# Performance work log

Measured on AMD Instinct MI355X. Metric: run time of the kernel, lower is better.

The kernel has to match this reference:

```python
import jax, jax.numpy as jnp
import numpy as np

B, S, D_MODEL, N_HEAD = 8, 512, 1024, 16
HEAD_DIM = D_MODEL // N_HEAD


def _pos_embed(seq_len, dim):
    # RelativeSinusoidalPositionalEmbedding(dim, padding_idx=0, init_size=1200)
    num = 1201  # init_size + 1
    half = dim // 2
    freq = np.exp(np.arange(half, dtype=np.float32) * (-np.log(10000.0) / (half - 1)))
    pos = np.arange(-((num + 1) // 2), num // 2, dtype=np.float32)  # tf.range(-num//2, num//2), python floor div
    emb = pos[:, None] * freq[None, :]
    table = np.concatenate([np.sin(emb), np.cos(emb)], axis=1).astype(np.float32)  # [num, dim]
    table[0] = 0.0  # padding_idx = 0
    origin_shift = num // 2 + 1  # 601
    idx = np.arange(-seq_len, seq_len) + origin_shift
    return jnp.asarray(table[idx])  # [2*seq_len, dim]


def setup_inputs() -> dict:
    key = jax.random.key(0)
    k1, k2, k3, k4 = jax.random.split(key, 4)
    return {
        "x": jax.random.normal(k1, (B, S, D_MODEL), dtype=jnp.float32),
        "mask": jnp.ones((B, S), dtype=jnp.int32),
        "Wqv": jax.random.normal(k2, (D_MODEL, 2 * D_MODEL), dtype=jnp.float32) * 0.02,
        "r_r_bias": jax.random.normal(k3, (N_HEAD, HEAD_DIM), dtype=jnp.float32) * 0.02,
        "r_w_bias": jax.random.normal(k4, (N_HEAD, HEAD_DIM), dtype=jnp.float32) * 0.02,
    }


def _shift(BD):
    # [b, h, s, 2s] -> [b, h, s, s] via pad-reshape trick
    b, h, s, _ = BD.shape
    zp = jnp.zeros((b, h, s, 1), BD.dtype)
    BD = jnp.concatenate([BD, zp], axis=-1).reshape(b, h, 2 * s + 1, s)
    BD = BD[:, :, :-1].reshape(b, h, s, 2 * s)
    return BD[:, :, :, s:]


def reference(x, mask, Wqv, r_r_bias, r_w_bias):
    pos = _pos_embed(S, HEAD_DIM)  # [2S, head_dim], stop-gradient constant
    qv = x @ Wqv  # [B, S, 2*D]
    q, v = jnp.split(qv, 2, axis=-1)

    def heads(t):
        return t.reshape(B, S, N_HEAD, HEAD_DIM).transpose(0, 2, 1, 3)  # bhsd

    q, k, v = heads(q), heads(x), heads(v)
    rw_q = q + r_r_bias[None, :, None, :]
    AC = jnp.einsum('bhqd,bhkd->bhqk', rw_q, k)
    D_ = jnp.einsum('hd,ld->hl', r_w_bias, pos)[None, :, None, :]  # [1, h, 1, 2S]
    B_ = jnp.einsum('bhqd,ld->bhql', q, pos)  # [b, h, S, 2S]
    BD = _shift(B_ + D_)
    attn = AC + BD  # scale=False -> divide by 1
    m = mask.astype(jnp.float32)[:, None, None, :]
    attn = attn * m - (1.0 - m) * 1e8
    attn = jax.nn.softmax(attn, axis=-1)  # dropout is identity at inference
    out = jnp.einsum('bhqk,bhkd->bhqd', attn, v)
    return out.transpose(0, 2, 1, 3).reshape(B, S, D_MODEL)
```

## Files before the change

### kernel.cpp

```cpp
#include <hip/hip_runtime.h>


using h4 = __attribute__((ext_vector_type(4))) _Float16;
using h8 = __attribute__((ext_vector_type(8))) _Float16;
using f32x4 = __attribute__((ext_vector_type(4))) float;

#define MFMA16(a, b, c) __builtin_amdgcn_mfma_f32_16x16x32_f16((a), (b), (c), 0, 0, 0)

#define GLOAD_LDS16(gp, lp)                                                        \
  __builtin_amdgcn_global_load_lds(                                                \
      (const __attribute__((address_space(1))) unsigned int*)(gp),                 \
      (__attribute__((address_space(3))) unsigned int*)(lp), 16, 0, 0)

#define L2E 1.4426950408889634f

__global__ __launch_bounds__(256) void k_prep(const float* __restrict__ x,
                                              const float* __restrict__ Wqv,
                                              _Float16* __restrict__ xh,
                                              _Float16* __restrict__ wT,
                                              _Float16* __restrict__ posP) {
  __shared__ _Float16 t[64][72];
  int bid = blockIdx.x;
  int tid = threadIdx.x;
  if (bid < 2048) {
    size_t idx = (size_t)bid * 256 + tid;
    const float* src = x + idx * 8;
    _Float16 tmp[8];
#pragma unroll
    for (int j = 0; j < 8; ++j) tmp[j] = (_Float16)src[j];
    *(h8*)(xh + idx * 8) = *(const h8*)tmp;
  } else if (bid < 2176) {
    int idx = (bid - 2048) * 256 + tid;
    int tt = idx >> 6, j = idx & 63;
    int jj = j & 31;
    float f = expf((float)jj * (-9.210340371976184f / 31.0f));
    float ang = (float)tt * f;
    posP[idx] = (_Float16)((j < 32) ? sinf(ang) : cosf(ang));
  } else {
    int b2 = bid - 2176;
    int bk = b2 & 15, bn = b2 >> 4;
    int k0 = bk * 64, n0 = bn * 64;
    int r = tid >> 2, c = (tid & 3) * 16;
    const float* src = Wqv + (size_t)(k0 + r) * 2048 + n0 + c;
#pragma unroll
    for (int j = 0; j < 16; ++j) t[r][c + j] = (_Float16)src[j];
    __syncthreads();
    _Float16 tmp[16];
#pragma unroll
    for (int j = 0; j < 16; ++j) tmp[j] = t[c + j][r];
    _Float16* dst = wT + (size_t)(n0 + r) * 1024 + k0 + c;
    *(h8*)dst = *(const h8*)tmp;
    *(h8*)(dst + 8) = *(const h8*)(tmp + 8);
  }
}

__global__ __launch_bounds__(256) void k_gemm(const _Float16* __restrict__ xh,
                                              const _Float16* __restrict__ wT,
                                              const float* __restrict__ rr,
                                              const float* __restrict__ rw,
                                              _Float16* __restrict__ qrr,
                                              _Float16* __restrict__ qrwp,
                                              _Float16* __restrict__ vT) {
  __shared__ _Float16 At[2][128 * 64];
  __shared__ _Float16 Bt[2][128 * 64];

  int bid = blockIdx.x;
  int bm = bid & 31, bn = bid >> 5;
  int tid = threadIdx.x;
  int w = tid >> 6, lane = tid & 63;
  int lr = lane & 15, lg = lane >> 4;

  auto stage = [&](int bufi, int k0) {
#pragma unroll
    for (int it = 0; it < 4; ++it) {
      int a = w * 256 + it * 64 + lane;
      int trow = a >> 3, c8s = (a & 7) ^ (trow & 7);
      GLOAD_LDS16(xh + (size_t)(bm * 128 + trow) * 1024 + k0 + c8s * 8,
                  &At[bufi][a * 8]);
    }
#pragma unroll
    for (int it = 0; it < 4; ++it) {
      int a = w * 256 + it * 64 + lane;
      int trow = a >> 3, c8s = (a & 7) ^ (trow & 7);
      GLOAD_LDS16(wT + (size_t)(bn * 128 + trow) * 1024 + k0 + c8s * 8,
                  &Bt[bufi][a * 8]);
    }
  };

  int wm = w >> 1, wn = w & 1;
  f32x4 acc[4][4] = {};

  stage(0, 0);
  __syncthreads();
  int buf = 0;
  for (int i = 0; i < 16; ++i) {
    if (i < 15) stage(buf ^ 1, (i + 1) * 64);
#pragma unroll
    for (int kk = 0; kk < 2; ++kk) {
      h8 af[4], bf[4];
#pragma unroll
      for (int mi = 0; mi < 4; ++mi) {
        int row = wm * 64 + mi * 16 + lr;
        af[mi] = *(const h8*)(&At[buf][row * 64 + (((kk * 4 + lg) ^ (lr & 7)) * 8)]);
      }
#pragma unroll
      for (int ni = 0; ni < 4; ++ni) {
        int row = wn * 64 + ni * 16 + lr;
        bf[ni] = *(const h8*)(&Bt[buf][row * 64 + (((kk * 4 + lg) ^ (lr & 7)) * 8)]);
      }
#pragma unroll
      for (int mi = 0; mi < 4; ++mi)
#pragma unroll
        for (int ni = 0; ni < 4; ++ni)
          acc[mi][ni] = MFMA16(af[mi], bf[ni], acc[mi][ni]);
    }
    __syncthreads();
    buf ^= 1;
  }

  int hg = bn * 2 + wn;
  int mb = bm * 128 + wm * 64;
  if (hg < 16) {
    int h = hg;
    float rrv[4], rwv[4];
#pragma unroll
    for (int ni = 0; ni < 4; ++ni) {
      rrv[ni] = rr[h * 64 + ni * 16 + lr];
      rwv[ni] = rw[h * 64 + ni * 16 + lr];
    }
    float f0 = expf((float)lr * (-9.210340371976184f / 31.0f));
    float f1 = expf((float)(16 + lr) * (-9.210340371976184f / 31.0f));
#pragma unroll
    for (int mi = 0; mi < 4; ++mi)
#pragma unroll
      for (int r = 0; r < 4; ++r) {
        int m = mb + mi * 16 + lg * 4 + r;
        int b = m >> 9, s = m & 511;
        size_t base = ((size_t)(b * 16 + h) * 512 + s) * 64;
#pragma unroll
        for (int ni = 0; ni < 4; ++ni)
          qrr[base + ni * 16 + lr] = (_Float16)((acc[mi][ni][r] + rrv[ni]) * L2E);
        {
          float qs = acc[mi][0][r] + rwv[0], qc = acc[mi][2][r] + rwv[2];
          float sn, cs;
          __sincosf((float)s * f0, &sn, &cs);
          qrwp[base + lr] = (_Float16)((qs * cs + qc * sn) * L2E);
          qrwp[base + lr + 32] = (_Float16)((qc * cs - qs * sn) * L2E);
        }
        {
          float qs = acc[mi][1][r] + rwv[1], qc = acc[mi][3][r] + rwv[3];
          float sn, cs;
          __sincosf((float)s * f1, &sn, &cs);
          qrwp[base + 16 + lr] = (_Float16)((qs * cs + qc * sn) * L2E);
          qrwp[base + 16 + lr + 32] = (_Float16)((qc * cs - qs * sn) * L2E);
        }
      }
  } else {
    int h = hg - 16;
#pragma unroll
    for (int mi = 0; mi < 4; ++mi) {
      int m = mb + mi * 16 + lg * 4;
      int b = m >> 9, s0 = m & 511;
      size_t vtbase = (size_t)(b * 16 + h) * 64 * 512;
#pragma unroll
      for (int ni = 0; ni < 4; ++ni) {
        int d = ni * 16 + lr;
        _Float16 t4[4];
#pragma unroll
        for (int r = 0; r < 4; ++r) t4[r] = (_Float16)acc[mi][ni][r];
        *(h4*)(vT + vtbase + (size_t)d * 512 + s0) = *(const h4*)t4;
      }
    }
  }
}

__global__ __launch_bounds__(256, 2) void k_attn(const _Float16* __restrict__ xh,
                                                 const _Float16* __restrict__ qrr,
                                                 const _Float16* __restrict__ qrwp,
                                                 const _Float16* __restrict__ vT,
                                                 const _Float16* __restrict__ posPg,
                                                 const int* __restrict__ mask,
                                                 float* __restrict__ out) {
  __shared__ _Float16 Kp[128 * 128];
  __shared__ _Float16 Vt[64 * 128];
  __shared__ _Float16 Pl[4][16 * 136];
  __shared__ float Ma[512];

  int bid = blockIdx.x;
  int qb = bid >> 7, h = bid & 15, b = (bid >> 4) & 7;
  int q0 = qb * 128;
  int tid = threadIdx.x;
  int w = tid >> 6, lane = tid & 63;
  int lr = lane & 15, lg = lane >> 4;

  const size_t bh = (size_t)(b * 16 + h);
  const _Float16* kb = xh + (size_t)b * 512 * 1024 + h * 64;
  const _Float16* vTp = vT + bh * 64 * 512;
  const int* mrow = mask + b * 512;

  auto stage = [&](int t0s) {
#pragma unroll
    for (int it = 0; it < 8; ++it) {
      int a = w * 512 + it * 64 + lane;
      int trow = a >> 4, c16 = a & 15;
      int c16s = c16 ^ (trow & 15);
      const _Float16* g = (c16s < 8)
          ? kb + (size_t)(t0s + trow) * 1024 + c16s * 8
          : posPg + (size_t)(t0s + trow) * 64 + (c16s - 8) * 8;
      GLOAD_LDS16(g, &Kp[(size_t)(w * 512 + it * 64) * 8]);
    }
#pragma unroll
    for (int it = 0; it < 4; ++it) {
      int a = w * 256 + it * 64 + lane;
      int drow = a >> 4, c16 = a & 15;
      int c16s = c16 ^ (drow & 15);
      const _Float16* g = vTp + (size_t)drow * 512 + t0s + c16s * 8;
      GLOAD_LDS16(g, &Vt[(size_t)(w * 256 + it * 64) * 8]);
    }
  };

  Ma[tid] = (1.f - (float)mrow[tid]) * -1.4426950e8f;
  Ma[tid + 256] = (1.f - (float)mrow[tid + 256]) * -1.4426950e8f;

  h8 ar0[2], ar1[2], aw0[2], aw1[2];
#pragma unroll
  for (int rg = 0; rg < 2; ++rg) {
    const _Float16* qrr_p = qrr + (bh * 512 + q0 + 32 * w + 16 * rg + lr) * 64 + lg * 8;
    const _Float16* qrw_p = qrwp + (bh * 512 + q0 + 32 * w + 16 * rg + lr) * 64 + lg * 8;
    ar0[rg] = *(const h8*)(qrr_p);
    ar1[rg] = *(const h8*)(qrr_p + 32);
    aw0[rg] = *(const h8*)(qrw_p);
    aw1[rg] = *(const h8*)(qrw_p + 32);
  }

  float m_run[2][4], l_run[2][4];
  f32x4 O[2][4];
#pragma unroll
  for (int rg = 0; rg < 2; ++rg)
#pragma unroll
    for (int r = 0; r < 4; ++r) {
      m_run[rg][r] = -1e30f;
      l_run[rg][r] = 0.f;
      O[rg][r] = (f32x4){0.f, 0.f, 0.f, 0.f};
    }

  _Float16* pw = &Pl[w][0];

  for (int t0 = 0; t0 < 512; t0 += 128) {
    stage(t0);
    __syncthreads();

#pragma unroll
    for (int rg = 0; rg < 2; ++rg) {
      float s[8][4];
      __builtin_amdgcn_s_setprio(1);
#pragma unroll
      for (int tf = 0; tf < 8; ++tf) {
        int row = tf * 16 + lr;
        const _Float16* bp = &Kp[row * 128];
        h8 b0 = *(const h8*)(bp + ((0 + lg) ^ lr) * 8);
        h8 b1 = *(const h8*)(bp + ((4 + lg) ^ lr) * 8);
        h8 b2 = *(const h8*)(bp + ((8 + lg) ^ lr) * 8);
        h8 b3 = *(const h8*)(bp + ((12 + lg) ^ lr) * 8);
        f32x4 c = {0.f, 0.f, 0.f, 0.f};
        c = MFMA16(ar0[rg], b0, c);
        c = MFMA16(ar1[rg], b1, c);
        c = MFMA16(aw0[rg], b2, c);
        c = MFMA16(aw1[rg], b3, c);
        float ma = Ma[t0 + tf * 16 + lr];
#pragma unroll
        for (int r = 0; r < 4; ++r) s[tf][r] = c[r] + ma;
      }
      __builtin_amdgcn_s_setprio(0);

#pragma unroll
      for (int r = 0; r < 4; ++r) {
        float rm = s[0][r];
#pragma unroll
        for (int tf = 1; tf < 8; ++tf) rm = fmaxf(rm, s[tf][r]);
#pragma unroll
        for (int d = 1; d < 16; d <<= 1) rm = fmaxf(rm, __shfl_xor(rm, d));
        float mn = fmaxf(m_run[rg][r], rm);
        float sc = exp2f(m_run[rg][r] - mn);
        m_run[rg][r] = mn;
        float rs = 0.f;
#pragma unroll
        for (int tf = 0; tf < 8; ++tf) {
          float p = exp2f(s[tf][r] - mn);
          _Float16 p16 = (_Float16)p;
          pw[(lg * 4 + r) * 136 + tf * 16 + lr] = p16;
          rs += (float)p16;
        }
#pragma unroll
        for (int d = 1; d < 16; d <<= 1) rs += __shfl_xor(rs, d);
        l_run[rg][r] = l_run[rg][r] * sc + rs;
#pragma unroll
        for (int df = 0; df < 4; ++df) O[rg][df][r] *= sc;
      }

      h8 pa[4];
#pragma unroll
      for (int ks = 0; ks < 4; ++ks)
        pa[ks] = *(const h8*)(pw + lr * 136 + ks * 32 + lg * 8);
      __builtin_amdgcn_s_setprio(1);
#pragma unroll
      for (int df = 0; df < 4; ++df) {
        int row = df * 16 + lr;
        const _Float16* vbp = &Vt[row * 128];
#pragma unroll
        for (int ks = 0; ks < 4; ++ks) {
          h8 vb = *(const h8*)(vbp + ((ks * 4 + lg) ^ lr) * 8);
          O[rg][df] = MFMA16(pa[ks], vb, O[rg][df]);
        }
      }
      __builtin_amdgcn_s_setprio(0);
    }
    __syncthreads();
  }

#pragma unroll
  for (int rg = 0; rg < 2; ++rg)
#pragma unroll
    for (int df = 0; df < 4; ++df)
#pragma unroll
      for (int r = 0; r < 4; ++r) {
        int ii = 32 * w + 16 * rg + lg * 4 + r;
        out[((size_t)b * 512 + q0 + ii) * 1024 + h * 64 + df * 16 + lr] =
            O[rg][df][r] / l_run[rg][r];
      }
}

extern "C" void kernel_launch(void* const* d_in, const int* in_sizes, int n_in,
                              void* d_out, int out_size, void* d_ws, size_t ws_size,
                              hipStream_t stream) {
  const float* x = (const float*)d_in[0];
  const int* mask = (const int*)d_in[1];
  const float* Wqv = (const float*)d_in[2];
  const float* rr = (const float*)d_in[3];
  const float* rw = (const float*)d_in[4];
  float* out = (float*)d_out;
  char* ws = (char*)d_ws;
  const size_t MB = 1024 * 1024;
  _Float16* xh = (_Float16*)(ws);
  _Float16* wT = (_Float16*)(ws + 8 * MB);
  _Float16* posP = (_Float16*)(ws + 12 * MB);
  _Float16* qrr = (_Float16*)(ws + 13 * MB);
  _Float16* qrwp = (_Float16*)(ws + 21 * MB);
  _Float16* vT = (_Float16*)(ws + 29 * MB);

  k_prep<<<2688, 256, 0, stream>>>(x, Wqv, xh, wT, posP);
  k_gemm<<<512, 256, 0, stream>>>(xh, wT, rr, rw, qrr, qrwp, vT);
  k_attn<<<512, 256, 0, stream>>>(xh, qrr, qrwp, vT, posP, mask, out);
}
```

Baseline: 72.23 us.

## Transpose QK MFMA so each lane owns a query row; add lazy softmax rescale

Swaps the MFMA operands so the score tile is transposed and each lane holds one query row's scores. Row max and sum then need only two cross-lane shuffles instead of four per register. It also skips the running-max rescale of O and l unless some row's max grows by more than 8 (log2 domain), and writes P as packed h4 stores. This cuts shuffle and exp work in the softmax, but the skipped rescale risks fp16 overflow of P if the threshold is too loose.

```diff
diff --git a/kernel.cpp b/kernel.cpp
--- a/kernel.cpp
+++ b/kernel.cpp
@@ -233,16 +233,12 @@
     aw1[rg] = *(const h8*)(qrw_p + 32);
   }
 
-  float m_run[2][4], l_run[2][4];
+  float m_run[2] = {-1e30f, -1e30f}, l_run[2] = {0.f, 0.f};
   f32x4 O[2][4];
 #pragma unroll
   for (int rg = 0; rg < 2; ++rg)
 #pragma unroll
-    for (int r = 0; r < 4; ++r) {
-      m_run[rg][r] = -1e30f;
-      l_run[rg][r] = 0.f;
-      O[rg][r] = (f32x4){0.f, 0.f, 0.f, 0.f};
-    }
+    for (int df = 0; df < 4; ++df) O[rg][df] = (f32x4){0.f, 0.f, 0.f, 0.f};
 
   _Float16* pw = &Pl[w][0];
 
@@ -263,40 +259,53 @@
         h8 b2 = *(const h8*)(bp + ((8 + lg) ^ lr) * 8);
         h8 b3 = *(const h8*)(bp + ((12 + lg) ^ lr) * 8);
         f32x4 c = {0.f, 0.f, 0.f, 0.f};
-        c = MFMA16(ar0[rg], b0, c);
-        c = MFMA16(ar1[rg], b1, c);
-        c = MFMA16(aw0[rg], b2, c);
-        c = MFMA16(aw1[rg], b3, c);
-        float ma = Ma[t0 + tf * 16 + lr];
-#pragma unroll
-        for (int r = 0; r < 4; ++r) s[tf][r] = c[r] + ma;
+        c = MFMA16(b0, ar0[rg], c);
+        c = MFMA16(b1, ar1[rg], c);
+        c = MFMA16(b2, aw0[rg], c);
+        c = MFMA16(b3, aw1[rg], c);
+        f32x4 mav = *(const f32x4*)&Ma[t0 + tf * 16 + lg * 4];
+#pragma unroll
+        for (int r = 0; r < 4; ++r) s[tf][r] = c[r] + mav[r];
       }
       __builtin_amdgcn_s_setprio(0);
 
-#pragma unroll
-      for (int r = 0; r < 4; ++r) {
-        float rm = s[0][r];
-#pragma unroll
-        for (int tf = 1; tf < 8; ++tf) rm = fmaxf(rm, s[tf][r]);
-#pragma unroll
-        for (int d = 1; d < 16; d <<= 1) rm = fmaxf(rm, __shfl_xor(rm, d));
-        float mn = fmaxf(m_run[rg][r], rm);
-        float sc = exp2f(m_run[rg][r] - mn);
-        m_run[rg][r] = mn;
-        float rs = 0.f;
-#pragma unroll
-        for (int tf = 0; tf < 8; ++tf) {
-          float p = exp2f(s[tf][r] - mn);
-          _Float16 p16 = (_Float16)p;
-          pw[(lg * 4 + r) * 136 + tf * 16 + lr] = p16;
-          rs += (float)p16;
+      float rm = s[0][0];
+#pragma unroll
+      for (int tf = 0; tf < 8; ++tf)
+#pragma unroll
+        for (int r = 0; r < 4; ++r) rm = fmaxf(rm, s[tf][r]);
+      rm = fmaxf(rm, __shfl_xor(rm, 16));
+      rm = fmaxf(rm, __shfl_xor(rm, 32));
+
+      if (!__all(rm - m_run[rg] <= 8.f)) {
+        float mn = fmaxf(m_run[rg], rm);
+        float sc = exp2f(m_run[rg] - mn);
+        m_run[rg] = mn;
+        l_run[rg] *= sc;
+        float scq[4];
+#pragma unroll
+        for (int r = 0; r < 4; ++r) scq[r] = __shfl(sc, lg * 4 + r);
+#pragma unroll
+        for (int df = 0; df < 4; ++df)
+#pragma unroll
+          for (int r = 0; r < 4; ++r) O[rg][df][r] *= scq[r];
+      }
+
+      float rs = 0.f;
+#pragma unroll
+      for (int tf = 0; tf < 8; ++tf) {
+        _Float16 p4[4];
+#pragma unroll
+        for (int r = 0; r < 4; ++r) {
+          float p = exp2f(s[tf][r] - m_run[rg]);
+          p4[r] = (_Float16)p;
+          rs += (float)p4[r];
         }
-#pragma unroll
-        for (int d = 1; d < 16; d <<= 1) rs += __shfl_xor(rs, d);
-        l_run[rg][r] = l_run[rg][r] * sc + rs;
-#pragma unroll
-        for (int df = 0; df < 4; ++df) O[rg][df][r] *= sc;
-      }
+        *(h4*)(pw + lr * 136 + tf * 16 + lg * 4) = *(const h4*)p4;
+      }
+      rs += __shfl_xor(rs, 16);
+      rs += __shfl_xor(rs, 32);
+      l_run[rg] += rs;
 
       h8 pa[4];
 #pragma unroll
@@ -319,15 +328,19 @@
   }
 
 #pragma unroll
-  for (int rg = 0; rg < 2; ++rg)
+  for (int rg = 0; rg < 2; ++rg) {
+    float lq[4];
+#pragma unroll
+    for (int r = 0; r < 4; ++r) lq[r] = __shfl(l_run[rg], lg * 4 + r);
 #pragma unroll
     for (int df = 0; df < 4; ++df)
 #pragma unroll
       for (int r = 0; r < 4; ++r) {
         int ii = 32 * w + 16 * rg + lg * 4 + r;
         out[((size_t)b * 512 + q0 + ii) * 1024 + h * 64 + df * 16 + lr] =
-            O[rg][df][r] / l_run[rg][r];
-      }
+            O[rg][df][r] / lq[r];
+      }
+  }
 }
 
 extern "C" void kernel_launch(void* const* d_in, const int* in_sizes, int n_in,
```

New measurement: 67.74 us (median of 3 runs). 1.07x faster.
